# Kernel tuning notes

Hardware: AMD Instinct MI355X
Metric: run time of the kernel (lower is better)

Reference implementation:

```python
import jax, jax.numpy as jnp
import numpy as np

LR = 0.01
EPS = 1e-8
D, H, O, N = 1024, 256, 64, 1024


def _normalize(W, b):
    # L2 (Frobenius) normalize weights and biases, clamped at EPS
    wn = jnp.maximum(jnp.sqrt(jnp.sum(W * W)), EPS)
    bn = jnp.maximum(jnp.sqrt(jnp.sum(b * b)), EPS)
    return W / wn, b / bn


def _step(carry, xt):
    W1, b1, W2, b2, W3, b3 = carry
    x, t = xt
    # forward pass (3-layer sigmoid MLP, softmax over -a3 as in original)
    a1 = jax.nn.sigmoid(x @ W1 + b1)
    a2 = jax.nn.sigmoid(a1 @ W2 + b2)
    a3 = jax.nn.sigmoid(a2 @ W3 + b3)
    out = jax.nn.softmax(-a3)
    # manual backprop deltas
    d3 = (t - out) * a3 * (1.0 - a3)
    o2 = (W3 @ d3) * a2 * (1.0 - a2)
    o1 = (W2 @ o2) * a1 * (1.0 - a1)
    # SGD update (note: original subtracts the delta, matching .sub_)
    W3 = W3 - LR * jnp.outer(a2, d3)
    b3 = b3 - LR * d3
    W2 = W2 - LR * jnp.outer(a1, o2)
    b2 = b2 - LR * o2
    W1 = W1 - LR * jnp.outer(x, o1)
    b1 = b1 - LR * o1
    # L2 normalize each layer's weights/biases
    W1, b1 = _normalize(W1, b1)
    W2, b2 = _normalize(W2, b2)
    W3, b3 = _normalize(W3, b3)
    return (W1, b1, W2, b2, W3, b3), None


def setup_inputs() -> dict:
    key = jax.random.key(0)
    k = jax.random.split(key, 5)
    return {
        "training_data": jax.random.normal(k[0], (N, D), jnp.float32),
        "training_targets": jax.random.uniform(k[1], (N, O), dtype=jnp.float32),
        "weights1": jax.random.normal(k[2], (D, H), jnp.float32) * 0.01,
        "biases1": jnp.zeros((H,), jnp.float32),
        "weights2": jax.random.normal(k[3], (H, H), jnp.float32) * 0.01,
        "biases2": jnp.zeros((H,), jnp.float32),
        "weights3": jax.random.normal(k[4], (H, O), jnp.float32) * 0.01,
        "biases3": jnp.zeros((O,), jnp.float32),
    }


def reference(training_data, training_targets, weights1, biases1, weights2, biases2, weights3, biases3):
    carry0 = (weights1, biases1, weights2, biases2, weights3, biases3)
    carry, _ = jax.lax.scan(_step, carry0, (training_data, training_targets))
    W1, b1, W2, b2, W3, b3 = carry
    return (W1, W2, W3)
```

## Files before the change

kernel.cpp:

```cpp
#include <hip/hip_runtime.h>
#include <math.h>


#define LRC  0.01f
#define EPSV 1e-8f

typedef float f32x8 __attribute__((ext_vector_type(8)));

#define SMEM_FLOATS 36400
#define SMEM_BYTES  (SMEM_FLOATS * 4)

#define ROWS16(OP)                                                            \
  OP(0) OP(1) OP(2) OP(3) OP(4) OP(5) OP(6) OP(7)                             \
  OP(8) OP(9) OP(10) OP(11) OP(12) OP(13) OP(14) OP(15)

__device__ __forceinline__ float hsum8(f32x8 v) {
  return ((v.s0 + v.s1) + (v.s2 + v.s3)) + ((v.s4 + v.s5) + (v.s6 + v.s7));
}

template <int CTRL>
__device__ __forceinline__ float dpp_add(float v) {
  const int s = __builtin_amdgcn_update_dpp(0, __builtin_bit_cast(int, v),
                                            CTRL, 0xf, 0xf, true);
  return v + __builtin_bit_cast(float, s);
}

__device__ __forceinline__ float dpp_allred64(float v) {
  v = dpp_add<0x111>(v);
  v = dpp_add<0x112>(v);
  v = dpp_add<0x114>(v);
  v = dpp_add<0x118>(v);
  v = dpp_add<0x142>(v);
  v = dpp_add<0x143>(v);
  return __builtin_bit_cast(float,
      __builtin_amdgcn_readlane(__builtin_bit_cast(int, v), 63));
}

__device__ __forceinline__ float wave_allred(float v) {
#pragma unroll
  for (int off = 32; off > 0; off >>= 1) v += __shfl_xor(v, off);
  return v;
}

__device__ __forceinline__ void wave_fence() {
  __builtin_amdgcn_sched_barrier(0);
  asm volatile("s_waitcnt lgkmcnt(0)" ::: "memory");
  __builtin_amdgcn_sched_barrier(0);
}

#define FMA16(c, a, b)                                                        \
  c[0][0] += a.x * b.x; c[0][1] += a.x * b.y; c[0][2] += a.x * b.z; c[0][3] += a.x * b.w; \
  c[1][0] += a.y * b.x; c[1][1] += a.y * b.y; c[1][2] += a.y * b.z; c[1][3] += a.y * b.w; \
  c[2][0] += a.z * b.x; c[2][1] += a.z * b.y; c[2][2] += a.z * b.z; c[2][3] += a.z * b.w; \
  c[3][0] += a.w * b.x; c[3][1] += a.w * b.y; c[3][2] += a.w * b.z; c[3][3] += a.w * b.w;

__global__ __launch_bounds__(256) void k_gram(const float* __restrict__ X,
                                              float* __restrict__ G) {
  const int bi = blockIdx.y, bj = blockIdx.x;
  if (bj > bi) return;
  __shared__ float Xa[32][68];
  __shared__ float Xb[32][68];
  const int tid = threadIdx.x;
  const int tx = tid & 15, ty = tid >> 4;
  float c[4][4] = {};
  for (int k0 = 0; k0 < 1024; k0 += 32) {
    __syncthreads();
    {
      const int row = tid >> 2, kk = (tid & 3) * 8;
      const float* pa = X + (bi * 64 + row) * 1024 + k0 + kk;
      const float4 a0 = *(const float4*)pa;
      const float4 a1 = *(const float4*)(pa + 4);
      Xa[kk + 0][row] = a0.x; Xa[kk + 1][row] = a0.y;
      Xa[kk + 2][row] = a0.z; Xa[kk + 3][row] = a0.w;
      Xa[kk + 4][row] = a1.x; Xa[kk + 5][row] = a1.y;
      Xa[kk + 6][row] = a1.z; Xa[kk + 7][row] = a1.w;
      const float* pb = X + (bj * 64 + row) * 1024 + k0 + kk;
      const float4 b0 = *(const float4*)pb;
      const float4 b1 = *(const float4*)(pb + 4);
      Xb[kk + 0][row] = b0.x; Xb[kk + 1][row] = b0.y;
      Xb[kk + 2][row] = b0.z; Xb[kk + 3][row] = b0.w;
      Xb[kk + 4][row] = b1.x; Xb[kk + 5][row] = b1.y;
      Xb[kk + 6][row] = b1.z; Xb[kk + 7][row] = b1.w;
    }
    __syncthreads();
#pragma unroll
    for (int kk = 0; kk < 32; kk++) {
      const float4 a = *(const float4*)&Xa[kk][ty * 4];
      const float4 b = *(const float4*)&Xb[kk][tx * 4];
      FMA16(c, a, b)
    }
  }
#pragma unroll
  for (int ii = 0; ii < 4; ii++) {
    *(float4*)(G + (bi * 64 + ty * 4 + ii) * 1024 + bj * 64 + tx * 4) =
        make_float4(c[ii][0], c[ii][1], c[ii][2], c[ii][3]);
  }
}

__global__ __launch_bounds__(256) void k_z10(const float* __restrict__ X,
                                             const float* __restrict__ W1g,
                                             float* __restrict__ Z10) {
  const int bi = blockIdx.y, bj = blockIdx.x;
  __shared__ float At[32][68];
  __shared__ float Bt[32][68];
  const int tid = threadIdx.x;
  const int tx = tid & 15, ty = tid >> 4;
  float c[4][4] = {};
  for (int k0 = 0; k0 < 1024; k0 += 32) {
    __syncthreads();
    {
      const int row = tid >> 2, kk = (tid & 3) * 8;
      const float* pa = X + (bi * 64 + row) * 1024 + k0 + kk;
      const float4 a0 = *(const float4*)pa;
      const float4 a1 = *(const float4*)(pa + 4);
      At[kk + 0][row] = a0.x; At[kk + 1][row] = a0.y;
      At[kk + 2][row] = a0.z; At[kk + 3][row] = a0.w;
      At[kk + 4][row] = a1.x; At[kk + 5][row] = a1.y;
      At[kk + 6][row] = a1.z; At[kk + 7][row] = a1.w;
      const int kr = tid >> 3, j8 = (tid & 7) * 8;
      const float* pb = W1g + (k0 + kr) * 256 + bj * 64 + j8;
      *(float4*)&Bt[kr][j8]     = *(const float4*)pb;
      *(float4*)&Bt[kr][j8 + 4] = *(const float4*)(pb + 4);
    }
    __syncthreads();
#pragma unroll
    for (int kk = 0; kk < 32; kk++) {
      const float4 a = *(const float4*)&At[kk][ty * 4];
      const float4 b = *(const float4*)&Bt[kk][tx * 4];
      FMA16(c, a, b)
    }
  }
#pragma unroll
  for (int ii = 0; ii < 4; ii++) {
    *(float4*)(Z10 + (bi * 64 + ty * 4 + ii) * 256 + bj * 64 + tx * 4) =
        make_float4(c[ii][0], c[ii][1], c[ii][2], c[ii][3]);
  }
}

__global__ __launch_bounds__(256) void k_w1out(
    const float* __restrict__ X, const float* __restrict__ o1g,
    const float* __restrict__ cg, const float* __restrict__ W1g,
    const float* __restrict__ sclg, float* __restrict__ outW1) {
  const int bi = blockIdx.y, bj = blockIdx.x;
  __shared__ float At[32][68];
  __shared__ float Bt[32][68];
  const int tid = threadIdx.x;
  const int tx = tid & 15, ty = tid >> 4;
  float c[4][4] = {};
  for (int k0 = 0; k0 < 1024; k0 += 32) {
    __syncthreads();
    {
      const int kr = tid >> 3, m8 = (tid & 7) * 8;
      const float* pa = X + (k0 + kr) * 1024 + bi * 64 + m8;
      *(float4*)&At[kr][m8]     = *(const float4*)pa;
      *(float4*)&At[kr][m8 + 4] = *(const float4*)(pa + 4);
      const float cs = cg[k0 + kr];
      const float* pb = o1g + (k0 + kr) * 256 + bj * 64 + m8;
      float4 b0 = *(const float4*)pb;
      float4 b1 = *(const float4*)(pb + 4);
      b0.x *= cs; b0.y *= cs; b0.z *= cs; b0.w *= cs;
      b1.x *= cs; b1.y *= cs; b1.z *= cs; b1.w *= cs;
      *(float4*)&Bt[kr][m8]     = b0;
      *(float4*)&Bt[kr][m8 + 4] = b1;
    }
    __syncthreads();
#pragma unroll
    for (int kk = 0; kk < 32; kk++) {
      const float4 a = *(const float4*)&At[kk][ty * 4];
      const float4 b = *(const float4*)&Bt[kk][tx * 4];
      FMA16(c, a, b)
    }
  }
  const float s1f = sclg[0];
#pragma unroll
  for (int ii = 0; ii < 4; ii++) {
    const int row = bi * 64 + ty * 4 + ii;
    const float4 w = *(const float4*)(W1g + row * 256 + bj * 64 + tx * 4);
    *(float4*)(outW1 + row * 256 + bj * 64 + tx * 4) =
        make_float4(s1f * (w.x + c[ii][0]), s1f * (w.y + c[ii][1]),
                    s1f * (w.z + c[ii][2]), s1f * (w.w + c[ii][3]));
  }
}

__device__ __forceinline__ float block_reduce8(float v, float* tmp, int tid) {
  v = wave_allred(v);
  __syncthreads();
  if ((tid & 63) == 0) tmp[tid >> 6] = v;
  __syncthreads();
  float s = 0.f;
#pragma unroll
  for (int w = 0; w < 8; w++) s += tmp[w];
  __syncthreads();
  return s;
}

__global__ __launch_bounds__(512, 1) void k2_seq(
    const float* __restrict__ Tg, const float* __restrict__ W1g,
    const float* __restrict__ b1g, const float* __restrict__ W2g,
    const float* __restrict__ b2g, const float* __restrict__ W3g,
    const float* __restrict__ b3g, const float* __restrict__ G,
    const float* __restrict__ Z10, float* __restrict__ o1g,
    float* __restrict__ cg, float* __restrict__ sclg,
    float* __restrict__ outW2, float* __restrict__ outW3) {
  extern __shared__ float sm[];
  float* const zo   = sm;
  float* const Gb   = sm + 17408;
  float* const scr  = sm + 21504;
  float* const Tb   = sm + 29952;
  float* const a1v  = sm + 34048;
  float* const z1v  = sm + 34560;
  float* const z2v  = sm + 34816;
  float* const a2v  = sm + 35072;
  float* const o2v  = sm + 35328;
  float* const b1ps = sm + 35584;
  float* const b2ps = sm + 35840;
  float* const d3v  = sm + 36096;
  float* const b3ps = sm + 36160;
  float* const ch   = sm + 36224;
  float* const dpart= sm + 36288;
  float* const sca  = sm + 36360;
  float* const cpre = sm + 36368;

  const int tid = threadIdx.x;
  const int lane = tid & 63;
  const int w = tid >> 6;
  const int p = tid >> 5;
  const int q = tid & 31;
  const int rown = 32 * w + (lane & 31);

  f32x8 W2_0, W2_1, W2_2, W2_3, W2_4, W2_5, W2_6, W2_7,
        W2_8, W2_9, W2_10, W2_11, W2_12, W2_13, W2_14, W2_15;
  float W3x_0, W3x_1, W3x_2, W3x_3, W3x_4, W3x_5, W3x_6, W3x_7,
        W3x_8, W3x_9, W3x_10, W3x_11, W3x_12, W3x_13, W3x_14, W3x_15;
  float W3y_0, W3y_1, W3y_2, W3y_3, W3y_4, W3y_5, W3y_6, W3y_7,
        W3y_8, W3y_9, W3y_10, W3y_11, W3y_12, W3y_13, W3y_14, W3y_15;

#define INIT_ROW(i)                                                           \
  { const int row = p * 16 + i;                                               \
    W2_##i  = *(const f32x8*)(W2g + row * 256 + q * 8);                       \
    W3x_##i = W3g[row * 64 + q * 2];                                          \
    W3y_##i = W3g[row * 64 + q * 2 + 1]; }
  ROWS16(INIT_ROW)

  if (tid < 256) {
    b1ps[tid] = b1g[tid]; b2ps[tid] = b2g[tid];
    o2v[tid] = 0.f;
    a1v[tid] = 0.f; a1v[256 + tid] = 0.f;
  }
  if (tid < 64) b3ps[tid] = b3g[tid];
  if (tid == 0) {
    sca[0] = 1.f; sca[1] = 1.f; sca[2] = 1.f; sca[3] = 1.f;
    sca[4] = 1.f; sca[5] = 1.f; sca[6] = 0.f; sca[7] = 0.f;
  }

  float acc1 = 0.f;
  for (int i = tid; i < 65536; i += 512) {
    const float4 v = ((const float4*)W1g)[i];
    acc1 += v.x * v.x + v.y * v.y + v.z * v.z + v.w * v.w;
  }
  const float n1init = block_reduce8(acc1, scr, tid);
  float acc2 = 0.f;
#define N2_ROW(i) { f32x8 t = W2_##i * W2_##i; acc2 += hsum8(t); }
  ROWS16(N2_ROW)
  const float n2init = block_reduce8(acc2, scr, tid);
  float acc3 = 0.f;
#define N3_ROW(i) acc3 += W3x_##i * W3x_##i + W3y_##i * W3y_##i;
  ROWS16(N3_ROW)
  const float n3init = block_reduce8(acc3, scr, tid);

  float s1 = 1.f, s2 = 1.f, s3 = 1.f;
  double n1d = (double)n1init;
  float n2 = n2init, n3 = n3init;
  __syncthreads();

  for (int b = 0; b < 16; b++) {
    const int bs = b * 64;
    {
      f32x8 pacc0 = {0.f, 0.f, 0.f, 0.f, 0.f, 0.f, 0.f, 0.f};
      f32x8 pacc1 = pacc0, pacc2 = pacc0, pacc3 = pacc0;
      for (int c0 = 0; c0 < bs; c0 += 32) {
        __syncthreads();
        if (tid < 32) cpre[tid] = cg[c0 + tid];
        {
          const int row = tid >> 3, k4 = (tid & 7) * 4;
          const float4 gv = *(const float4*)(G + (bs + row) * 1024 + c0 + k4);
          Gb[row * 33 + k4 + 0] = gv.x; Gb[row * 33 + k4 + 1] = gv.y;
          Gb[row * 33 + k4 + 2] = gv.z; Gb[row * 33 + k4 + 3] = gv.w;
        }
#pragma unroll
        for (int u = 0; u < 4; u++) {
          const int fi = tid + u * 512;
          ((float4*)scr)[fi] = ((const float4*)(o1g + c0 * 256))[fi];
        }
        __syncthreads();
#pragma unroll 2
        for (int ss = 0; ss < 32; ss++) {
          const float cs = cpre[ss];
          const f32x8 o8 = *(const f32x8*)(scr + ss * 256 + q * 8);
          pacc0 += (Gb[(p * 4 + 0) * 33 + ss] * cs) * o8;
          pacc1 += (Gb[(p * 4 + 1) * 33 + ss] * cs) * o8;
          pacc2 += (Gb[(p * 4 + 2) * 33 + ss] * cs) * o8;
          pacc3 += (Gb[(p * 4 + 3) * 33 + ss] * cs) * o8;
        }
      }
      __syncthreads();
#define ZSTORE(rr)                                                            \
      { const int row = p * 4 + rr;                                           \
        *(f32x8*)(zo + row * 272 + q * 8) =                                   \
            *(const f32x8*)(Z10 + (bs + row) * 256 + q * 8) + pacc##rr; }
      ZSTORE(0) ZSTORE(1) ZSTORE(2) ZSTORE(3)
#pragma unroll
      for (int u = 0; u < 2; u++) {
        const int fi = tid + u * 512;
        const int row = fi >> 4, c4 = fi & 15;
        *(float4*)(Gb + row * 64 + c4 * 4) =
            *(const float4*)(G + (bs + row) * 1024 + bs + c4 * 4);
      }
      ((float4*)Tb)[tid]       = ((const float4*)(Tg + bs * 64))[tid];
      ((float4*)Tb)[tid + 512] = ((const float4*)(Tg + bs * 64))[tid + 512];
      __syncthreads();
    }

    for (int l = 0; l < 64; l++) {
      const int t = bs + l;
      const int cur = (t & 1) * 256, prv = 256 - cur;
      const float s1c = sca[0], rb1c = sca[1], s2c = sca[2], rb2c = sca[3],
                  s3c = sca[4], rb3c = sca[5], cw2c = sca[6], cw3c = sca[7];

#define W2_UPD()                                                              \
      { const f32x8 o8s = cw2c * (*(const f32x8*)&o2v[q * 8]);                \
        const float* apv = &a1v[prv + p * 16];                                \
        W2_0  += apv[0]  * o8s; W2_1  += apv[1]  * o8s;                       \
        W2_2  += apv[2]  * o8s; W2_3  += apv[3]  * o8s;                       \
        W2_4  += apv[4]  * o8s; W2_5  += apv[5]  * o8s;                       \
        W2_6  += apv[6]  * o8s; W2_7  += apv[7]  * o8s;                       \
        W2_8  += apv[8]  * o8s; W2_9  += apv[9]  * o8s;                       \
        W2_10 += apv[10] * o8s; W2_11 += apv[11] * o8s;                       \
        W2_12 += apv[12] * o8s; W2_13 += apv[13] * o8s;                       \
        W2_14 += apv[14] * o8s; W2_15 += apv[15] * o8s; }

      if (t > 0) {
        const float d0s = cw3c * d3v[q * 2], d1s = cw3c * d3v[q * 2 + 1];
#define UPD3_ROW(i)                                                           \
        { const float a2o = a2v[p * 16 + i];                                  \
          W3x_##i += a2o * d0s; W3y_##i += a2o * d1s; }
        ROWS16(UPD3_ROW)
      }
      {
        const int jp = tid >> 2, quarter = tid & 3;
        float ax = 0.f, ay = 0.f;
        for (int lp = quarter; lp < l; lp += 4) {
          const float gcs = ch[lp] * Gb[l * 64 + lp];
          const float2 zr = *(const float2*)&zo[lp * 272 + 2 * jp];
          ax += gcs * zr.x; ay += gcs * zr.y;
        }
        ax = dpp_add<0xB1>(ax); ax = dpp_add<0x4E>(ax);
        ay = dpp_add<0xB1>(ay); ay = dpp_add<0x4E>(ay);
        const float2 zop = *(const float2*)&zo[l * 272 + 2 * jp];
        const float2 b1q = *(const float2*)&b1ps[2 * jp];
        const float2 ap  = *(const float2*)&a1v[prv + 2 * jp];
        const float z1u0 = zop.x + ax, z1u1 = zop.y + ay;
        const float a1x0 = 1.f / (1.f + expf(-(s1c * z1u0 + rb1c * b1q.x)));
        const float a1x1 = 1.f / (1.f + expf(-(s1c * z1u1 + rb1c * b1q.y)));
        if (quarter == 0) {
          *(float2*)&z1v[2 * jp] = make_float2(z1u0, z1u1);
          *(float2*)&a1v[cur + 2 * jp] = make_float2(a1x0, a1x1);
        }
        const float v3 = dpp_allred64(
            quarter == 0 ? a1x0 * a1x0 + a1x1 * a1x1 : 0.f);
        const float vad = dpp_allred64(
            quarter == 0 ? a1x0 * ap.x + a1x1 * ap.y : 0.f);
        if (lane == 0) { dpart[48 + w] = v3; dpart[56 + w] = vad; }
      }
      __syncthreads();

      {
        f32x8 acc = {0.f, 0.f, 0.f, 0.f, 0.f, 0.f, 0.f, 0.f};
#define B1_ROW(i) acc += a1v[cur + p * 16 + i] * W2_##i;
        ROWS16(B1_ROW)
        *(f32x8*)&scr[p * 264 + q * 8] = acc;
      }
      __syncthreads();

      if (tid < 256) {
        float s = 0.f;
#pragma unroll
        for (int pp = 0; pp < 16; pp++) s += scr[pp * 264 + tid];
        const float adot = ((dpart[56] + dpart[57]) + (dpart[58] + dpart[59]))
                         + ((dpart[60] + dpart[61]) + (dpart[62] + dpart[63]));
        const float z2p = s2c * (s + cw2c * adot * o2v[tid]);
        z2v[tid] = z2p;
        const float a2x = 1.f / (1.f + expf(-(z2p + rb2c * b2ps[tid])));
        a2v[tid] = a2x;
        const float v6 = dpp_allred64(a2x * a2x);
        if ((tid & 63) == 0) dpart[64 + (tid >> 6)] = v6;
      } else if (t > 0) {
        W2_UPD()
      }
      __syncthreads();

      {
        float c0a = 0.f, c1a = 0.f;
#define C1_ROW(i)                                                             \
        { const float a2x = a2v[p * 16 + i];                                  \
          c0a += a2x * W3x_##i; c1a += a2x * W3y_##i; }
        ROWS16(C1_ROW)
        scr[(q * 2 + 0) * 17 + p] = c0a;
        scr[(q * 2 + 1) * 17 + p] = c1a;
      }
      __syncthreads();

      if (w == 7) {
        float s = 0.f;
#pragma unroll
        for (int pp = 0; pp < 16; pp++) s += scr[lane * 17 + pp];
        const float z3p = s3c * s;
        const float a3 = 1.f / (1.f + expf(-(z3p + rb3c * b3ps[lane])));
        const float e = expf(-a3);
        const float tot = dpp_allred64(e);
        const float outv = e / tot;
        const float d3 = (Tb[l * 64 + lane] - outv) * a3 * (1.f - a3);
        d3v[lane] = d3;
        const float b3n = rb3c * b3ps[lane] - LRC * d3;
        b3ps[lane] = b3n;
        const float v5 = dpp_allred64(z3p * d3);
        const float v7 = dpp_allred64(d3 * d3);
        const float v10 = dpp_allred64(b3n * b3n);
        if (lane == 0) { dpart[68] = v5; dpart[69] = v7; dpart[70] = v10; }
      } else if (w < 4 && t > 0) {
        W2_UPD()
      }
      __syncthreads();

      {
        const float d0 = d3v[q * 2 + 0], d1 = d3v[q * 2 + 1];
#define E1_ROW(i) scr[(p * 16 + i) * 33 + q] = W3x_##i * d0 + W3y_##i * d1;
        ROWS16(E1_ROW)
        wave_fence();
        float s = 0.f;
#pragma unroll
        for (int qq = 0; qq < 32; qq++) s += scr[rown * 33 + qq];
        const float a2x = a2v[rown];
        const float o2x = s3c * s * a2x * (1.f - a2x);
        const float b2n = rb2c * b2ps[rown] - LRC * o2x;
        const bool own = (lane & 32) == 0;
        if (own) { o2v[rown] = o2x; b2ps[rown] = b2n; }
        const float v2 = dpp_allred64(own ? z2v[rown] * o2x : 0.f);
        const float v4 = dpp_allred64(own ? o2x * o2x : 0.f);
        const float v9 = dpp_allred64(own ? b2n * b2n : 0.f);
        if (lane == 0) {
          dpart[24 + w] = v2; dpart[32 + w] = v4; dpart[40 + w] = v9;
        }
      }
      __syncthreads();

      {
        const f32x8 ov8 = *(const f32x8*)&o2v[q * 8];
#define F_ROW(i)                                                              \
        { f32x8 tq = W2_##i * ov8; scr[(p * 16 + i) * 33 + q] = hsum8(tq); }
        ROWS16(F_ROW)
        wave_fence();
        float s = 0.f;
#pragma unroll
        for (int qq = 0; qq < 32; qq++) s += scr[rown * 33 + qq];
        const float a1x = a1v[cur + rown];
        const float o1x = s2c * s * a1x * (1.f - a1x);
        const float b1n = rb1c * b1ps[rown] - LRC * o1x;
        const float z1x = z1v[rown];
        const bool own = (lane & 32) == 0;
        if (own) { zo[l * 272 + rown] = o1x; b1ps[rown] = b1n; }
        const float v0 = dpp_allred64(own ? z1x * o1x : 0.f);
        const float v1 = dpp_allred64(own ? o1x * o1x : 0.f);
        const float v8 = dpp_allred64(own ? b1n * b1n : 0.f);
        if (lane == 0) {
          dpart[0 + w] = v0; dpart[8 + w] = v1; dpart[16 + w] = v8;
        }
      }
      __syncthreads();

      if (w == 0) {
        const float dts0 = ((dpart[0] + dpart[1]) + (dpart[2] + dpart[3]))
                         + ((dpart[4] + dpart[5]) + (dpart[6] + dpart[7]));
        const float dts1 = ((dpart[8] + dpart[9]) + (dpart[10] + dpart[11]))
                         + ((dpart[12] + dpart[13]) + (dpart[14] + dpart[15]));
        const float dts8 = ((dpart[16] + dpart[17]) + (dpart[18] + dpart[19]))
                         + ((dpart[20] + dpart[21]) + (dpart[22] + dpart[23]));
        const float c1 = -LRC / s1;
        const double gtt = (double)Gb[l * 65];
        n1d = n1d + 2.0 * (double)c1 * (double)dts0 +
              (double)c1 * (double)c1 * gtt * (double)dts1;
        const double w1n = (double)s1 * sqrt(n1d);
        s1 = (float)((double)s1 / fmax(w1n, (double)EPSV));
        if (lane == 0) {
          ch[l] = c1;
          sca[0] = s1;
          sca[1] = 1.f / fmaxf(sqrtf(dts8), EPSV);
        }
      } else if (w == 7) {
        const float dts2 = ((dpart[24] + dpart[25]) + (dpart[26] + dpart[27]))
                         + ((dpart[28] + dpart[29]) + (dpart[30] + dpart[31]));
        const float dts4 = ((dpart[32] + dpart[33]) + (dpart[34] + dpart[35]))
                         + ((dpart[36] + dpart[37]) + (dpart[38] + dpart[39]));
        const float dts9 = ((dpart[40] + dpart[41]) + (dpart[42] + dpart[43]))
                         + ((dpart[44] + dpart[45]) + (dpart[46] + dpart[47]));
        const float dts3 = ((dpart[48] + dpart[49]) + (dpart[50] + dpart[51]))
                         + ((dpart[52] + dpart[53]) + (dpart[54] + dpart[55]));
        const float dts6 = (dpart[64] + dpart[65]) + (dpart[66] + dpart[67]);
        const float dts5 = dpart[68], dts7 = dpart[69], dts10 = dpart[70];
        const float n2p = n2 - 2.f * LRC * dts2 + LRC * LRC * dts3 * dts4;
        const float r2s = 1.f / fmaxf(sqrtf(n2p), EPSV);
        n2 = n2p * r2s * r2s;
        const float cw2n = -LRC / s2;
        s2 = s2 * r2s;
        const float n3p = n3 - 2.f * LRC * dts5 + LRC * LRC * dts6 * dts7;
        const float r3s = 1.f / fmaxf(sqrtf(n3p), EPSV);
        n3 = n3p * r3s * r3s;
        const float cw3n = -LRC / s3;
        s3 = s3 * r3s;
        if (lane == 0) {
          sca[2] = s2;
          sca[3] = 1.f / fmaxf(sqrtf(dts9), EPSV);
          sca[4] = s3;
          sca[5] = 1.f / fmaxf(sqrtf(dts10), EPSV);
          sca[6] = cw2n;
          sca[7] = cw3n;
        }
      }
      __syncthreads();
    }

    {
#pragma unroll
      for (int u = 0; u < 4; u++) {
        const int chunk = tid + u * 512;
        const int row = chunk >> 5, c8 = chunk & 31;
        *(f32x8*)(o1g + (bs + row) * 256 + c8 * 8) =
            *(const f32x8*)(zo + row * 272 + c8 * 8);
      }
      if (tid < 64) cg[bs + tid] = ch[tid];
    }
  }

  {
    const float cw2f = sca[6], cw3f = sca[7];
    const float s2f = sca[2], s3f = sca[4];
    const f32x8 o8s = cw2f * (*(const f32x8*)&o2v[q * 8]);
    const float d0s = cw3f * d3v[q * 2], d1s = cw3f * d3v[q * 2 + 1];
#define FIN_ROW(i)                                                            \
    { const float a1o = a1v[256 + p * 16 + i];          \
      W2_##i += a1o * o8s;                                                    \
      const float a2o = a2v[p * 16 + i];                                      \
      W3x_##i += a2o * d0s; W3y_##i += a2o * d1s;                             \
      const int row = p * 16 + i;                                             \
      *(f32x8*)(outW2 + row * 256 + q * 8) = s2f * W2_##i;                    \
      outW3[row * 64 + q * 2]     = s3f * W3x_##i;                            \
      outW3[row * 64 + q * 2 + 1] = s3f * W3y_##i; }
    ROWS16(FIN_ROW)
    if (tid == 0) sclg[0] = sca[0];
  }
}

extern "C" void kernel_launch(void* const* d_in, const int* in_sizes, int n_in,
                              void* d_out, int out_size, void* d_ws,
                              size_t ws_size, hipStream_t stream) {
  (void)in_sizes; (void)n_in; (void)out_size; (void)ws_size;
  const float* X   = (const float*)d_in[0];
  const float* Tg  = (const float*)d_in[1];
  const float* W1g = (const float*)d_in[2];
  const float* b1g = (const float*)d_in[3];
  const float* W2g = (const float*)d_in[4];
  const float* b2g = (const float*)d_in[5];
  const float* W3g = (const float*)d_in[6];
  const float* b3g = (const float*)d_in[7];
  float* out = (float*)d_out;
  float* ws  = (float*)d_ws;

  float* G    = ws;
  float* Z10  = G + 1048576;
  float* o1g  = Z10 + 262144;
  float* cg   = o1g + 262144;
  float* sclg = cg + 1024;

  (void)hipFuncSetAttribute((const void*)k2_seq,
                            hipFuncAttributeMaxDynamicSharedMemorySize,
                            SMEM_BYTES);

  k_gram<<<dim3(16, 16), 256, 0, stream>>>(X, G);
  k_z10<<<dim3(4, 16), 256, 0, stream>>>(X, W1g, Z10);
  k2_seq<<<dim3(1), dim3(512), SMEM_BYTES, stream>>>(
      Tg, W1g, b1g, W2g, b2g, W3g, b3g, G, Z10, o1g, cg, sclg,
      out + 262144, out + 327680);
  k_w1out<<<dim3(4, 16), 256, 0, stream>>>(X, o1g, cg, W1g, sclg, out);
}
```

Baseline: 8.657 ms.

## Replace per-step block barriers with LDS flag spins and defer scalar chains

The per-step scalar norm updates run by waves 0 and 7 no longer sit behind a trailing __syncthreads. They move to the start of the next step and publish their results through LDS flags, which other waves spin on only just before they need the scalars. The layer-3 softmax wave likewise signals by flag instead of a full barrier. o2v and the dpart partials are double-buffered so the deferred work does not race with the current step. The aim is to shorten the serial critical path per timestep by cutting barriers and overlapping the scalar chains with the G·z accumulation. The cost is busy-wait spinning and extra care needed around LDS memory ordering.

```diff
diff --git a/kernel.cpp b/kernel.cpp
--- a/kernel.cpp
+++ b/kernel.cpp
@@ -7,7 +7,7 @@
 
 typedef float f32x8 __attribute__((ext_vector_type(8)));
 
-#define SMEM_FLOATS 36400
+#define SMEM_FLOATS 37768
 #define SMEM_BYTES  (SMEM_FLOATS * 4)
 
 #define ROWS16(OP)                                                            \
@@ -46,6 +46,10 @@
   __builtin_amdgcn_sched_barrier(0);
   asm volatile("s_waitcnt lgkmcnt(0)" ::: "memory");
   __builtin_amdgcn_sched_barrier(0);
+}
+
+__device__ __forceinline__ void lds_spin(volatile int* f, int want) {
+  while (*f != want) {}
 }
 
 #define FMA16(c, a, b)                                                        \
@@ -194,6 +198,9 @@
   return s;
 }
 
+#define SUM8(x0, x1) (((x0.x + x0.y) + (x0.z + x0.w)) +                       \
+                      ((x1.x + x1.y) + (x1.z + x1.w)))
+
 __global__ __launch_bounds__(512, 1) void k2_seq(
     const float* __restrict__ Tg, const float* __restrict__ W1g,
     const float* __restrict__ b1g, const float* __restrict__ W2g,
@@ -212,14 +219,17 @@
   float* const z2v  = sm + 34816;
   float* const a2v  = sm + 35072;
   float* const o2v  = sm + 35328;
-  float* const b1ps = sm + 35584;
-  float* const b2ps = sm + 35840;
-  float* const d3v  = sm + 36096;
-  float* const b3ps = sm + 36160;
-  float* const ch   = sm + 36224;
-  float* const dpart= sm + 36288;
-  float* const sca  = sm + 36360;
-  float* const cpre = sm + 36368;
+  float* const b1ps = sm + 35840;
+  float* const b2ps = sm + 36096;
+  float* const d3v  = sm + 36352;
+  float* const b3ps = sm + 36416;
+  float* const ch   = sm + 36480;
+  float* const dpart= sm + 36544;
+  float* const sca  = sm + 36632;
+  float* const cpre = sm + 36644;
+  float* const csc  = sm + 36676;
+  int*   const flgi = (int*)(sm + 37764);
+
 
   const int tid = threadIdx.x;
   const int lane = tid & 63;
@@ -244,13 +254,14 @@
 
   if (tid < 256) {
     b1ps[tid] = b1g[tid]; b2ps[tid] = b2g[tid];
-    o2v[tid] = 0.f;
+    o2v[tid] = 0.f; o2v[256 + tid] = 0.f;
     a1v[tid] = 0.f; a1v[256 + tid] = 0.f;
   }
   if (tid < 64) b3ps[tid] = b3g[tid];
   if (tid == 0) {
     sca[0] = 1.f; sca[1] = 1.f; sca[2] = 1.f; sca[3] = 1.f;
-    sca[4] = 1.f; sca[5] = 1.f; sca[6] = 0.f; sca[7] = 0.f;
+    sca[4] = 1.f; sca[5] = 1.f; sca[6] = 0.f; sca[7] = 0.f; sca[8] = 0.f;
+    flgi[0] = -1; flgi[1] = -1; flgi[2] = -1;
   }
 
   float acc1 = 0.f;
@@ -272,6 +283,65 @@
   double n1d = (double)n1init;
   float n2 = n2init, n3 = n3init;
   __syncthreads();
+
+  auto chain0 = [&](const int lidx) {
+    const float4 qa0 = *(const float4*)&dpart[0];
+    const float4 qa1 = *(const float4*)&dpart[4];
+    const float4 qb0 = *(const float4*)&dpart[8];
+    const float4 qb1 = *(const float4*)&dpart[12];
+    const float4 qc0 = *(const float4*)&dpart[16];
+    const float4 qc1 = *(const float4*)&dpart[20];
+    const float dts0 = SUM8(qa0, qa1);
+    const float dts1 = SUM8(qb0, qb1);
+    const float dts8 = SUM8(qc0, qc1);
+    const float c1 = -LRC / s1;
+    const double gtt = (double)Gb[lidx * 65];
+    n1d = n1d + 2.0 * (double)c1 * (double)dts0 +
+          (double)c1 * (double)c1 * gtt * (double)dts1;
+    const double w1n = (double)s1 * sqrt(n1d);
+    s1 = (float)((double)s1 / fmax(w1n, (double)EPSV));
+    if (lane == 0) {
+      ch[lidx] = c1;
+      sca[0] = s1;
+      sca[1] = 1.f / fmaxf(sqrtf(dts8), EPSV);
+      sca[8] = c1;
+    }
+  };
+  auto chain7 = [&](const int par) {
+    const float4 qd0 = *(const float4*)&dpart[24];
+    const float4 qd1 = *(const float4*)&dpart[28];
+    const float4 qe0 = *(const float4*)&dpart[32];
+    const float4 qe1 = *(const float4*)&dpart[36];
+    const float4 qf0 = *(const float4*)&dpart[40];
+    const float4 qf1 = *(const float4*)&dpart[44];
+    const float4 qg0 = *(const float4*)&dpart[48 + par * 8];
+    const float4 qg1 = *(const float4*)&dpart[52 + par * 8];
+    const float4 qh  = *(const float4*)&dpart[80];
+    const float dts2 = SUM8(qd0, qd1);
+    const float dts4 = SUM8(qe0, qe1);
+    const float dts9 = SUM8(qf0, qf1);
+    const float dts3 = SUM8(qg0, qg1);
+    const float dts6 = (qh.x + qh.y) + (qh.z + qh.w);
+    const float dts5 = dpart[84], dts7 = dpart[85], dts10 = dpart[86];
+    const float n2p = n2 - 2.f * LRC * dts2 + LRC * LRC * dts3 * dts4;
+    const float r2s = 1.f / fmaxf(sqrtf(n2p), EPSV);
+    n2 = n2p * r2s * r2s;
+    const float cw2n = -LRC / s2;
+    s2 = s2 * r2s;
+    const float n3p = n3 - 2.f * LRC * dts5 + LRC * LRC * dts6 * dts7;
+    const float r3s = 1.f / fmaxf(sqrtf(n3p), EPSV);
+    n3 = n3p * r3s * r3s;
+    const float cw3n = -LRC / s3;
+    s3 = s3 * r3s;
+    if (lane == 0) {
+      sca[2] = s2;
+      sca[3] = 1.f / fmaxf(sqrtf(dts9), EPSV);
+      sca[4] = s3;
+      sca[5] = 1.f / fmaxf(sqrtf(dts10), EPSV);
+      sca[6] = cw2n;
+      sca[7] = cw3n;
+    }
+  };
 
   for (int b = 0; b < 16; b++) {
     const int bs = b * 64;
@@ -324,11 +394,10 @@
     for (int l = 0; l < 64; l++) {
       const int t = bs + l;
       const int cur = (t & 1) * 256, prv = 256 - cur;
-      const float s1c = sca[0], rb1c = sca[1], s2c = sca[2], rb2c = sca[3],
-                  s3c = sca[4], rb3c = sca[5], cw2c = sca[6], cw3c = sca[7];
 
 #define W2_UPD()                                                              \
-      { const f32x8 o8s = cw2c * (*(const f32x8*)&o2v[q * 8]);                \
+      { const float cw2u = sca[6];                                            \
+        const f32x8 o8s = cw2u * (*(const f32x8*)&o2v[prv + q * 8]);          \
         const float* apv = &a1v[prv + p * 16];                                \
         W2_0  += apv[0]  * o8s; W2_1  += apv[1]  * o8s;                       \
         W2_2  += apv[2]  * o8s; W2_3  += apv[3]  * o8s;                       \
@@ -339,19 +408,34 @@
         W2_12 += apv[12] * o8s; W2_13 += apv[13] * o8s;                       \
         W2_14 += apv[14] * o8s; W2_15 += apv[15] * o8s; }
 
-      if (t > 0) {
-        const float d0s = cw3c * d3v[q * 2], d1s = cw3c * d3v[q * 2 + 1];
-#define UPD3_ROW(i)                                                           \
-        { const float a2o = a2v[p * 16 + i];                                  \
-          W3x_##i += a2o * d0s; W3y_##i += a2o * d1s; }
-        ROWS16(UPD3_ROW)
+      if (l > 0) {
+        if (w == 0) {
+          chain0(l - 1);
+          wave_fence();
+          if (lane == 0) *(volatile int*)&flgi[0] = t;
+        } else if (w == 7) {
+          chain7((t - 1) & 1);
+          wave_fence();
+          if (lane == 0) *(volatile int*)&flgi[1] = t;
+        }
       }
       {
         const int jp = tid >> 2, quarter = tid & 3;
         float ax = 0.f, ay = 0.f;
-        for (int lp = quarter; lp < l; lp += 4) {
+        for (int lp = quarter; lp < l - 1; lp += 4) {
           const float gcs = ch[lp] * Gb[l * 64 + lp];
           const float2 zr = *(const float2*)&zo[lp * 272 + 2 * jp];
+          ax += gcs * zr.x; ay += gcs * zr.y;
+        }
+        if (l > 0) {
+          if (w != 0) lds_spin(&flgi[0], t);
+          if (w != 7) lds_spin(&flgi[1], t);
+        }
+        asm volatile("" ::: "memory");
+        const float s1c = sca[0], rb1c = sca[1];
+        if (l > 0 && ((l - 1) & 3) == quarter) {
+          const float gcs = sca[8] * Gb[l * 64 + (l - 1)];
+          const float2 zr = *(const float2*)&zo[(l - 1) * 272 + 2 * jp];
           ax += gcs * zr.x; ay += gcs * zr.y;
         }
         ax = dpp_add<0xB1>(ax); ax = dpp_add<0x4E>(ax);
@@ -370,7 +454,18 @@
             quarter == 0 ? a1x0 * a1x0 + a1x1 * a1x1 : 0.f);
         const float vad = dpp_allred64(
             quarter == 0 ? a1x0 * ap.x + a1x1 * ap.y : 0.f);
-        if (lane == 0) { dpart[48 + w] = v3; dpart[56 + w] = vad; }
+        if (lane == 0) {
+          dpart[48 + (t & 1) * 8 + w] = v3;
+          dpart[64 + w] = vad;
+        }
+      }
+      if (t > 0) {
+        const float cw3c = sca[7];
+        const float d0s = cw3c * d3v[q * 2], d1s = cw3c * d3v[q * 2 + 1];
+#define UPD3_ROW(i)                                                           \
+        { const float a2o = a2v[p * 16 + i];                                  \
+          W3x_##i += a2o * d0s; W3y_##i += a2o * d1s; }
+        ROWS16(UPD3_ROW)
       }
       __syncthreads();
 
@@ -383,17 +478,18 @@
       __syncthreads();
 
       if (tid < 256) {
+        const float s2c = sca[2], rb2c = sca[3], cw2c = sca[6];
         float s = 0.f;
 #pragma unroll
         for (int pp = 0; pp < 16; pp++) s += scr[pp * 264 + tid];
-        const float adot = ((dpart[56] + dpart[57]) + (dpart[58] + dpart[59]))
-                         + ((dpart[60] + dpart[61]) + (dpart[62] + dpart[63]));
-        const float z2p = s2c * (s + cw2c * adot * o2v[tid]);
+        const float adot = ((dpart[64] + dpart[65]) + (dpart[66] + dpart[67]))
+                         + ((dpart[68] + dpart[69]) + (dpart[70] + dpart[71]));
+        const float z2p = s2c * (s + cw2c * adot * o2v[prv + tid]);
         z2v[tid] = z2p;
         const float a2x = 1.f / (1.f + expf(-(z2p + rb2c * b2ps[tid])));
         a2v[tid] = a2x;
         const float v6 = dpp_allred64(a2x * a2x);
-        if ((tid & 63) == 0) dpart[64 + (tid >> 6)] = v6;
+        if ((tid & 63) == 0) dpart[80 + (tid >> 6)] = v6;
       } else if (t > 0) {
         W2_UPD()
       }
@@ -405,34 +501,40 @@
         { const float a2x = a2v[p * 16 + i];                                  \
           c0a += a2x * W3x_##i; c1a += a2x * W3y_##i; }
         ROWS16(C1_ROW)
-        scr[(q * 2 + 0) * 17 + p] = c0a;
-        scr[(q * 2 + 1) * 17 + p] = c1a;
-      }
-      __syncthreads();
-
-      if (w == 7) {
-        float s = 0.f;
-#pragma unroll
-        for (int pp = 0; pp < 16; pp++) s += scr[lane * 17 + pp];
-        const float z3p = s3c * s;
-        const float a3 = 1.f / (1.f + expf(-(z3p + rb3c * b3ps[lane])));
-        const float e = expf(-a3);
-        const float tot = dpp_allred64(e);
-        const float outv = e / tot;
-        const float d3 = (Tb[l * 64 + lane] - outv) * a3 * (1.f - a3);
-        d3v[lane] = d3;
-        const float b3n = rb3c * b3ps[lane] - LRC * d3;
-        b3ps[lane] = b3n;
-        const float v5 = dpp_allred64(z3p * d3);
-        const float v7 = dpp_allred64(d3 * d3);
-        const float v10 = dpp_allred64(b3n * b3n);
-        if (lane == 0) { dpart[68] = v5; dpart[69] = v7; dpart[70] = v10; }
-      } else if (w < 4 && t > 0) {
-        W2_UPD()
+        csc[(q * 2 + 0) * 17 + p] = c0a;
+        csc[(q * 2 + 1) * 17 + p] = c1a;
       }
       __syncthreads();
 
       {
+        if (w == 7) {
+          const float s3c = sca[4], rb3c = sca[5];
+          float s = 0.f;
+#pragma unroll
+          for (int pp = 0; pp < 16; pp++) s += csc[lane * 17 + pp];
+          const float z3p = s3c * s;
+          const float a3 = 1.f / (1.f + expf(-(z3p + rb3c * b3ps[lane])));
+          const float e = expf(-a3);
+          const float tot = dpp_allred64(e);
+          const float outv = e / tot;
+          const float d3 = (Tb[l * 64 + lane] - outv) * a3 * (1.f - a3);
+          d3v[lane] = d3;
+          const float b3n = rb3c * b3ps[lane] - LRC * d3;
+          b3ps[lane] = b3n;
+          const float v5 = dpp_allred64(z3p * d3);
+          const float v7 = dpp_allred64(d3 * d3);
+          const float v10 = dpp_allred64(b3n * b3n);
+          if (lane == 0) { dpart[84] = v5; dpart[85] = v7; dpart[86] = v10; }
+          wave_fence();
+          if (lane == 0) *(volatile int*)&flgi[2] = t;
+        } else if (w < 4) {
+          if (t > 0) { W2_UPD() }
+          lds_spin((volatile int*)&flgi[2], t);
+        } else {
+          lds_spin((volatile int*)&flgi[2], t);
+        }
+        asm volatile("" ::: "memory");
+        const float s3c = sca[4], rb2c = sca[3];
         const float d0 = d3v[q * 2 + 0], d1 = d3v[q * 2 + 1];
 #define E1_ROW(i) scr[(p * 16 + i) * 33 + q] = W3x_##i * d0 + W3y_##i * d1;
         ROWS16(E1_ROW)
@@ -444,7 +546,7 @@
         const float o2x = s3c * s * a2x * (1.f - a2x);
         const float b2n = rb2c * b2ps[rown] - LRC * o2x;
         const bool own = (lane & 32) == 0;
-        if (own) { o2v[rown] = o2x; b2ps[rown] = b2n; }
+        if (own) { o2v[cur + rown] = o2x; b2ps[rown] = b2n; }
         const float v2 = dpp_allred64(own ? z2v[rown] * o2x : 0.f);
         const float v4 = dpp_allred64(own ? o2x * o2x : 0.f);
         const float v9 = dpp_allred64(own ? b2n * b2n : 0.f);
@@ -455,7 +557,8 @@
       __syncthreads();
 
       {
-        const f32x8 ov8 = *(const f32x8*)&o2v[q * 8];
+        const float s2c = sca[2], rb1c = sca[1];
+        const f32x8 ov8 = *(const f32x8*)&o2v[cur + q * 8];
 #define F_ROW(i)                                                              \
         { f32x8 tq = W2_##i * ov8; scr[(p * 16 + i) * 33 + q] = hsum8(tq); }
         ROWS16(F_ROW)
@@ -477,57 +580,11 @@
         }
       }
       __syncthreads();
-
-      if (w == 0) {
-        const float dts0 = ((dpart[0] + dpart[1]) + (dpart[2] + dpart[3]))
-                         + ((dpart[4] + dpart[5]) + (dpart[6] + dpart[7]));
-        const float dts1 = ((dpart[8] + dpart[9]) + (dpart[10] + dpart[11]))
-                         + ((dpart[12] + dpart[13]) + (dpart[14] + dpart[15]));
-        const float dts8 = ((dpart[16] + dpart[17]) + (dpart[18] + dpart[19]))
-                         + ((dpart[20] + dpart[21]) + (dpart[22] + dpart[23]));
-        const float c1 = -LRC / s1;
-        const double gtt = (double)Gb[l * 65];
-        n1d = n1d + 2.0 * (double)c1 * (double)dts0 +
-              (double)c1 * (double)c1 * gtt * (double)dts1;
-        const double w1n = (double)s1 * sqrt(n1d);
-        s1 = (float)((double)s1 / fmax(w1n, (double)EPSV));
-        if (lane == 0) {
-          ch[l] = c1;
-          sca[0] = s1;
-          sca[1] = 1.f / fmaxf(sqrtf(dts8), EPSV);
-        }
-      } else if (w == 7) {
-        const float dts2 = ((dpart[24] + dpart[25]) + (dpart[26] + dpart[27]))
-                         + ((dpart[28] + dpart[29]) + (dpart[30] + dpart[31]));
-        const float dts4 = ((dpart[32] + dpart[33]) + (dpart[34] + dpart[35]))
-                         + ((dpart[36] + dpart[37]) + (dpart[38] + dpart[39]));
-        const float dts9 = ((dpart[40] + dpart[41]) + (dpart[42] + dpart[43]))
-                         + ((dpart[44] + dpart[45]) + (dpart[46] + dpart[47]));
-        const float dts3 = ((dpart[48] + dpart[49]) + (dpart[50] + dpart[51]))
-                         + ((dpart[52] + dpart[53]) + (dpart[54] + dpart[55]));
-        const float dts6 = (dpart[64] + dpart[65]) + (dpart[66] + dpart[67]);
-        const float dts5 = dpart[68], dts7 = dpart[69], dts10 = dpart[70];
-        const float n2p = n2 - 2.f * LRC * dts2 + LRC * LRC * dts3 * dts4;
-        const float r2s = 1.f / fmaxf(sqrtf(n2p), EPSV);
-        n2 = n2p * r2s * r2s;
-        const float cw2n = -LRC / s2;
-        s2 = s2 * r2s;
-        const float n3p = n3 - 2.f * LRC * dts5 + LRC * LRC * dts6 * dts7;
-        const float r3s = 1.f / fmaxf(sqrtf(n3p), EPSV);
-        n3 = n3p * r3s * r3s;
-        const float cw3n = -LRC / s3;
-        s3 = s3 * r3s;
-        if (lane == 0) {
-          sca[2] = s2;
-          sca[3] = 1.f / fmaxf(sqrtf(dts9), EPSV);
-          sca[4] = s3;
-          sca[5] = 1.f / fmaxf(sqrtf(dts10), EPSV);
-          sca[6] = cw2n;
-          sca[7] = cw3n;
-        }
-      }
-      __syncthreads();
-    }
+    }
+
+    if (w == 0) chain0(63);
+    else if (w == 7) chain7((bs + 63) & 1);
+    __syncthreads();
 
     {
 #pragma unroll
@@ -544,10 +601,10 @@
   {
     const float cw2f = sca[6], cw3f = sca[7];
     const float s2f = sca[2], s3f = sca[4];
-    const f32x8 o8s = cw2f * (*(const f32x8*)&o2v[q * 8]);
+    const f32x8 o8s = cw2f * (*(const f32x8*)&o2v[256 + q * 8]);
     const float d0s = cw3f * d3v[q * 2], d1s = cw3f * d3v[q * 2 + 1];
 #define FIN_ROW(i)                                                            \
-    { const float a1o = a1v[256 + p * 16 + i];          \
+    { const float a1o = a1v[256 + p * 16 + i];                                \
       W2_##i += a1o * o8s;                                                    \
       const float a2o = a2v[p * 16 + i];                                      \
       W3x_##i += a2o * d0s; W3y_##i += a2o * d1s;                             \
```

Result: faster. 8.475 ms (-2.1%).
